# Performance work log

Hardware: AMD Instinct MI355X
Metric: run time of the kernel (lower is better)

The kernel has to match this reference:

```python
import jax, jax.numpy as jnp
import numpy as np

# ---- static config (mirrors build() with the chosen init_kwargs) ----
B, H, W, C = 16, 56, 56, 128
KH, KW = 3, 3          # filter_size
SH, SW = 1, 1          # stride
NF = 256               # n_filters
IN_FEAT = C * KH * KW  # 1152
NNZ = int(1 * 0.2 * IN_FEAT * NF)  # multiple * density * n_parameters = 58982


def _make_indices():
    """Replicates the full='output' sparsity-pattern construction from build()."""
    rng = np.random.default_rng(0)
    per_col = NNZ // NF
    remain = NNZ % NF
    remain_cols = set(rng.choice(NF, remain, replace=False).tolist())
    chunks = []
    for col in rng.permutation(NF):
        k = per_col + (1 if int(col) in remain_cols else 0)
        rows = rng.choice(IN_FEAT, k, replace=False)
        chunks.append(np.stack([rows, np.full(k, col, dtype=np.int64)], axis=1))
    return np.concatenate(chunks, axis=0).astype(np.int32)  # (NNZ, 2) [row, col]


def setup_inputs() -> dict:
    key = jax.random.key(0)
    k1, k2 = jax.random.split(key)
    x = jax.random.normal(k1, (B, H, W, C), dtype=jnp.float32)
    limit = float(np.sqrt(6.0 / (IN_FEAT + NF)))  # glorot_uniform on the sparse values
    kernel = jax.random.uniform(k2, (NNZ,), jnp.float32, -limit, limit)
    bias = jnp.zeros((NF,), jnp.float32)
    indices = jnp.asarray(_make_indices())
    return {"x": x, "kernel": kernel, "bias": bias, "indices": indices}


def _im2col_valid(x):
    # tf.image.extract_patches ordering: patch positions row-major (di, dj),
    # channels fastest -> concatenate C-channel slices in (di, dj) order.
    oh = (H - KH) // SH + 1
    ow = (W - KW) // SW + 1
    cols = [x[:, di:di + oh * SH:SH, dj:dj + ow * SW:SW, :]
            for di in range(KH) for dj in range(KW)]
    return jnp.concatenate(cols, axis=-1), oh, ow  # (B, oh, ow, IN_FEAT)


def reference(x, kernel, bias, indices):
    patches, oh, ow = _im2col_valid(x)
    pm = patches.reshape(-1, IN_FEAT)  # (B*oh*ow, IN_FEAT)
    # Sparse (IN_FEAT, NF) weight: scatter values into a dense matrix
    # (indices are unique by construction, so .add == .set and is grad-safe).
    Wm = jnp.zeros((IN_FEAT, NF), dtype=pm.dtype).at[indices[:, 0], indices[:, 1]].add(kernel)
    out = pm @ Wm + bias            # sparse-dense matmul + bias
    out = jax.nn.relu(out)          # activation
    return out.reshape(B, oh, ow, NF)
```

## Files before the change

kernel.cpp:

```cpp
#include <hip/hip_runtime.h>

typedef unsigned short u16;
typedef __bf16 bf16x8 __attribute__((ext_vector_type(8)));
typedef float f32x4 __attribute__((ext_vector_type(4)));

#define B_   16
#define H_   56
#define W_   56
#define C_   128
#define OH_  54
#define OW_  54
#define NF_  256
#define KF_  1152
#define M_   46656
#define NNZ_ 58982

#define XB_ELEMS (B_*H_*W_*C_)
#define WT_ELEMS (36*4*256*8)

__device__ __forceinline__ u16 f2bf(float f) {
    unsigned u = __float_as_uint(f);
    u += 0x7FFFu + ((u >> 16) & 1u);
    return (u16)(u >> 16);
}

__device__ __forceinline__ void gload16(const void* g, void* l) {
    __builtin_amdgcn_global_load_lds(
        (const __attribute__((address_space(1))) unsigned int*)g,
        (__attribute__((address_space(3))) unsigned int*)l,
        16, 0, 0);
}

__global__ __launch_bounds__(256) void cvt_x_kernel(const float* __restrict__ x,
                                                    u16* __restrict__ xb) {
    int i = (blockIdx.x * 256 + threadIdx.x) * 8;
    float4 v0 = *(const float4*)(x + i);
    float4 v1 = *(const float4*)(x + i + 4);
    union { u16 u[8]; uint4 v; } r;
    r.u[0] = f2bf(v0.x); r.u[1] = f2bf(v0.y); r.u[2] = f2bf(v0.z); r.u[3] = f2bf(v0.w);
    r.u[4] = f2bf(v1.x); r.u[5] = f2bf(v1.y); r.u[6] = f2bf(v1.z); r.u[7] = f2bf(v1.w);
    *(uint4*)(xb + i) = r.v;
}

__global__ __launch_bounds__(256) void scatter_kernel(const float* __restrict__ kv,
                                                      const int* __restrict__ idx,
                                                      u16* __restrict__ wt) {
    int t = blockIdx.x * 256 + threadIdx.x;
    if (t >= NNZ_) return;
    int k   = idx[2*t];
    int col = idx[2*t + 1];
    int kt = k >> 5, ks = (k >> 3) & 3, e = k & 7;
    wt[(kt * 4 + ks) * 2048 + col * 8 + e] = f2bf(kv[t]);
}

__global__ __launch_bounds__(256) void spconv_gemm(const u16* __restrict__ xb,
                                                   const u16* __restrict__ wt,
                                                   const float* __restrict__ bias,
                                                   float* __restrict__ out) {
    __shared__ __align__(16) u16 As[2][64 * 32];
    __shared__ __align__(16) u16 Bs[2][4 * 256 * 8];

    const int t    = threadIdx.x;
    const int lane = t & 63;
    const int wid  = t >> 6;

    const int nwg = gridDim.x;
    const int q = nwg >> 3, r = nwg & 7;
    const int xcd = blockIdx.x & 7, inner = blockIdx.x >> 3;
    const int wg = (xcd < r ? xcd * (q + 1) : r * (q + 1) + (xcd - r) * q) + inner;
    const int m0 = wg * 64;

    const int arow = (wid << 4) | (lane >> 2);
    const int kc   = lane & 3;
    const int kcs  = kc ^ (arow & 3) ^ ((arow >> 2) & 3);
    const int kco  = kcs * 8;
    int mg  = m0 + arow;
    int bb  = mg / (OH_ * OW_);
    int rem = mg % (OH_ * OW_);
    int ii  = rem / OW_;
    int jj  = rem % OW_;
    const u16* a_base = xb + ((bb * H_ + ii) * W_ + jj) * C_;
    const int a_dst = t * 8;
    const int b_dst = t * 8;

    f32x4 acc[4][4];
    const f32x4 zz = {0.f, 0.f, 0.f, 0.f};
#pragma unroll
    for (int i = 0; i < 4; ++i)
#pragma unroll
        for (int j = 0; j < 4; ++j) acc[i][j] = zz;

    const int ks  = lane >> 4;
    const int r16 = lane & 15;
    const int cidx = ks ^ (r16 & 3) ^ ((r16 >> 2) & 3);

#define ISSUE(kn, bi) do {                                                  \
    int g_  = (kn) >> 2;                                                    \
    int di_ = (g_ * 11) >> 5;                                               \
    int dj_ = g_ - 3 * di_;                                                 \
    int aoff_ = (di_ * W_ + dj_) * C_ + ((kn) & 3) * 32 + kco;              \
    gload16(a_base + aoff_, &As[bi][0] + a_dst);                            \
    const u16* bsrc_ = wt + (kn) * 8192 + t * 8;                            \
    gload16(bsrc_,        &Bs[bi][0] + b_dst);                              \
    gload16(bsrc_ + 2048, &Bs[bi][0] + b_dst + 2048);                       \
    gload16(bsrc_ + 4096, &Bs[bi][0] + b_dst + 4096);                       \
    gload16(bsrc_ + 6144, &Bs[bi][0] + b_dst + 6144);                       \
} while (0)

#define COMPUTE(bi) do {                                                    \
    bf16x8 a_[4], b_[4];                                                    \
    _Pragma("unroll")                                                       \
    for (int mf = 0; mf < 4; ++mf)                                          \
        a_[mf] = *(const bf16x8*)(&As[bi][(mf * 16 + r16) * 32 + cidx * 8]);\
    _Pragma("unroll")                                                       \
    for (int nf = 0; nf < 4; ++nf)                                          \
        b_[nf] = *(const bf16x8*)(&Bs[bi][(ks * 256 + wid * 64 + nf * 16 + r16) * 8]); \
    _Pragma("unroll")                                                       \
    for (int mf = 0; mf < 4; ++mf)                                          \
        _Pragma("unroll")                                                   \
        for (int nf = 0; nf < 4; ++nf)                                      \
            acc[mf][nf] = __builtin_amdgcn_mfma_f32_16x16x32_bf16(          \
                a_[mf], b_[nf], acc[mf][nf], 0, 0, 0);                      \
} while (0)

#define WAITVM(n) asm volatile("s_waitcnt vmcnt(" #n ")" ::: "memory")
#define BAR() do { __builtin_amdgcn_s_barrier();                            \
                   asm volatile("" ::: "memory"); } while (0)

    ISSUE(0, 0);
    ISSUE(1, 1);

#pragma unroll
    for (int k = 0; k < 34; ++k) {
        WAITVM(5);
        BAR();
        COMPUTE(k & 1);
        BAR();
        ISSUE(k + 2, k & 1);
    }
    WAITVM(5); BAR(); COMPUTE(0); BAR();
    WAITVM(0); BAR(); COMPUTE(1);

#undef ISSUE
#undef COMPUTE
#undef WAITVM
#undef BAR

    const int rgrp = lane >> 4;
#pragma unroll
    for (int nf = 0; nf < 4; ++nf) {
        int col  = wid * 64 + nf * 16 + r16;
        float bv = bias[col];
#pragma unroll
        for (int mf = 0; mf < 4; ++mf) {
#pragma unroll
            for (int rr = 0; rr < 4; ++rr) {
                int row = m0 + mf * 16 + rgrp * 4 + rr;
                float v = acc[mf][nf][rr] + bv;
                out[row * NF_ + col] = fmaxf(v, 0.f);
            }
        }
    }
}

extern "C" void kernel_launch(void* const* d_in, const int* in_sizes, int n_in,
                              void* d_out, int out_size, void* d_ws, size_t ws_size,
                              hipStream_t stream) {
    const float* x    = (const float*)d_in[0];
    const float* kv   = (const float*)d_in[1];
    const float* bias = (const float*)d_in[2];
    const int*   idx  = (const int*)d_in[3];
    float* out = (float*)d_out;

    u16* xb  = (u16*)d_ws;
    u16* wtp = (u16*)((char*)d_ws + (size_t)XB_ELEMS * 2);

    hipMemsetAsync(wtp, 0, (size_t)WT_ELEMS * 2, stream);
    cvt_x_kernel<<<XB_ELEMS / (256 * 8), 256, 0, stream>>>(x, xb);
    scatter_kernel<<<(NNZ_ + 255) / 256, 256, 0, stream>>>(kv, idx, wtp);
    spconv_gemm<<<M_ / 64, 256, 0, stream>>>(xb, wtp, bias, out);
}
```

Measured before the change: 50.70 us.

## Enlarge GEMM tile to 96 rows with 6 waves and warp-specialized loaders; fuse memset

```diff
diff --git a/kernel.cpp b/kernel.cpp
--- a/kernel.cpp
+++ b/kernel.cpp
@@ -32,7 +32,12 @@
 }
 
 __global__ __launch_bounds__(256) void cvt_x_kernel(const float* __restrict__ x,
-                                                    u16* __restrict__ xb) {
+                                                    u16* __restrict__ xb,
+                                                    u16* __restrict__ wt) {
+    if (blockIdx.x < 144) {
+        uint4 z = {0u, 0u, 0u, 0u};
+        ((uint4*)wt)[blockIdx.x * 256 + threadIdx.x] = z;
+    }
     int i = (blockIdx.x * 256 + threadIdx.x) * 8;
     float4 v0 = *(const float4*)(x + i);
     float4 v1 = *(const float4*)(x + i + 4);
@@ -53,11 +58,11 @@
     wt[(kt * 4 + ks) * 2048 + col * 8 + e] = f2bf(kv[t]);
 }
 
-__global__ __launch_bounds__(256) void spconv_gemm(const u16* __restrict__ xb,
+__global__ __launch_bounds__(384) void spconv_gemm(const u16* __restrict__ xb,
                                                    const u16* __restrict__ wt,
                                                    const float* __restrict__ bias,
                                                    float* __restrict__ out) {
-    __shared__ __align__(16) u16 As[2][64 * 32];
+    __shared__ __align__(16) u16 As[2][96 * 32];
     __shared__ __align__(16) u16 Bs[2][4 * 256 * 8];
 
     const int t    = threadIdx.x;
@@ -68,62 +73,79 @@
     const int q = nwg >> 3, r = nwg & 7;
     const int xcd = blockIdx.x & 7, inner = blockIdx.x >> 3;
     const int wg = (xcd < r ? xcd * (q + 1) : r * (q + 1) + (xcd - r) * q) + inner;
-    const int m0 = wg * 64;
-
-    const int arow = (wid << 4) | (lane >> 2);
-    const int kc   = lane & 3;
-    const int kcs  = kc ^ (arow & 3) ^ ((arow >> 2) & 3);
-    const int kco  = kcs * 8;
-    int mg  = m0 + arow;
-    int bb  = mg / (OH_ * OW_);
-    int rem = mg % (OH_ * OW_);
-    int ii  = rem / OW_;
-    int jj  = rem % OW_;
-    const u16* a_base = xb + ((bb * H_ + ii) * W_ + jj) * C_;
-    const int a_dst = t * 8;
-    const int b_dst = t * 8;
-
-    f32x4 acc[4][4];
+    const int m0 = wg * 96;
+
+    const int u     = t & 127;
+    const int arow0 = u >> 2;
+    const int kc    = u & 3;
+    const int kcs   = kc ^ (arow0 & 3) ^ ((arow0 >> 2) & 3);
+    const int kco   = kcs * 8;
+    const int a_dst0 = u * 8;
+
+    const u16* a_base0;
+    const u16* a_base1;
+    const u16* a_base2;
+    {
+        int mg0 = m0 + arow0;
+#define MKBASE(dst, mg) do {                                   \
+        int bb_  = (mg) / (OH_ * OW_);                         \
+        int rem_ = (mg) % (OH_ * OW_);                         \
+        int ii_  = rem_ / OW_;                                 \
+        int jj_  = rem_ % OW_;                                 \
+        dst = xb + ((bb_ * H_ + ii_) * W_ + jj_) * C_;         \
+    } while (0)
+        MKBASE(a_base0, mg0);
+        MKBASE(a_base1, mg0 + 32);
+        MKBASE(a_base2, mg0 + 64);
+#undef MKBASE
+    }
+
+    f32x4 acc[2][8];
     const f32x4 zz = {0.f, 0.f, 0.f, 0.f};
 #pragma unroll
-    for (int i = 0; i < 4; ++i)
-#pragma unroll
-        for (int j = 0; j < 4; ++j) acc[i][j] = zz;
+    for (int i = 0; i < 2; ++i)
+#pragma unroll
+        for (int j = 0; j < 8; ++j) acc[i][j] = zz;
 
     const int ks  = lane >> 4;
     const int r16 = lane & 15;
     const int cidx = ks ^ (r16 & 3) ^ ((r16 >> 2) & 3);
+    const int wr = wid >> 1;
+    const int wc = wid & 1;
 
 #define ISSUE(kn, bi) do {                                                  \
-    int g_  = (kn) >> 2;                                                    \
-    int di_ = (g_ * 11) >> 5;                                               \
-    int dj_ = g_ - 3 * di_;                                                 \
-    int aoff_ = (di_ * W_ + dj_) * C_ + ((kn) & 3) * 32 + kco;              \
-    gload16(a_base + aoff_, &As[bi][0] + a_dst);                            \
-    const u16* bsrc_ = wt + (kn) * 8192 + t * 8;                            \
-    gload16(bsrc_,        &Bs[bi][0] + b_dst);                              \
-    gload16(bsrc_ + 2048, &Bs[bi][0] + b_dst + 2048);                       \
-    gload16(bsrc_ + 4096, &Bs[bi][0] + b_dst + 4096);                       \
-    gload16(bsrc_ + 6144, &Bs[bi][0] + b_dst + 6144);                       \
+    if (t < 256) {                                                          \
+        const u16* bsrc_ = wt + (kn) * 8192 + t * 8;                        \
+        gload16(bsrc_,        &Bs[bi][0] + t * 8);                          \
+        gload16(bsrc_ + 2048, &Bs[bi][0] + t * 8 + 2048);                   \
+        gload16(bsrc_ + 4096, &Bs[bi][0] + t * 8 + 4096);                   \
+        gload16(bsrc_ + 6144, &Bs[bi][0] + t * 8 + 6144);                   \
+    } else {                                                                \
+        int g_  = (kn) >> 2;                                                \
+        int di_ = (g_ * 11) >> 5;                                           \
+        int dj_ = g_ - 3 * di_;                                             \
+        int aoff_ = (di_ * W_ + dj_) * C_ + ((kn) & 3) * 32 + kco;          \
+        gload16(a_base0 + aoff_, &As[bi][0] + a_dst0);                      \
+        gload16(a_base1 + aoff_, &As[bi][0] + a_dst0 + 1024);               \
+        gload16(a_base2 + aoff_, &As[bi][0] + a_dst0 + 2048);               \
+    }                                                                       \
 } while (0)
 
 #define COMPUTE(bi) do {                                                    \
-    bf16x8 a_[4], b_[4];                                                    \
+    bf16x8 a0_ = *(const bf16x8*)(&As[bi][(wr * 32 + r16) * 32 + cidx * 8]);\
+    bf16x8 a1_ = *(const bf16x8*)(&As[bi][(wr * 32 + 16 + r16) * 32 + cidx * 8]); \
     _Pragma("unroll")                                                       \
-    for (int mf = 0; mf < 4; ++mf)                                          \
-        a_[mf] = *(const bf16x8*)(&As[bi][(mf * 16 + r16) * 32 + cidx * 8]);\
-    _Pragma("unroll")                                                       \
-    for (int nf = 0; nf < 4; ++nf)                                          \
-        b_[nf] = *(const bf16x8*)(&Bs[bi][(ks * 256 + wid * 64 + nf * 16 + r16) * 8]); \
-    _Pragma("unroll")                                                       \
-    for (int mf = 0; mf < 4; ++mf)                                          \
-        _Pragma("unroll")                                                   \
-        for (int nf = 0; nf < 4; ++nf)                                      \
-            acc[mf][nf] = __builtin_amdgcn_mfma_f32_16x16x32_bf16(          \
-                a_[mf], b_[nf], acc[mf][nf], 0, 0, 0);                      \
+    for (int nf = 0; nf < 8; ++nf) {                                        \
+        bf16x8 b_ = *(const bf16x8*)(&Bs[bi][(ks * 256 + wc * 128 + nf * 16 + r16) * 8]); \
+        acc[0][nf] = __builtin_amdgcn_mfma_f32_16x16x32_bf16(a0_, b_, acc[0][nf], 0, 0, 0); \
+        acc[1][nf] = __builtin_amdgcn_mfma_f32_16x16x32_bf16(a1_, b_, acc[1][nf], 0, 0, 0); \
+    }                                                                       \
 } while (0)
 
-#define WAITVM(n) asm volatile("s_waitcnt vmcnt(" #n ")" ::: "memory")
+#define WAITVM(nb, na) do {                                                 \
+    if (wid < 4) { asm volatile("s_waitcnt vmcnt(" #nb ")" ::: "memory"); } \
+    else         { asm volatile("s_waitcnt vmcnt(" #na ")" ::: "memory"); } \
+} while (0)
 #define BAR() do { __builtin_amdgcn_s_barrier();                            \
                    asm volatile("" ::: "memory"); } while (0)
 
@@ -132,14 +154,14 @@
 
 #pragma unroll
     for (int k = 0; k < 34; ++k) {
-        WAITVM(5);
+        WAITVM(4, 3);
         BAR();
         COMPUTE(k & 1);
         BAR();
         ISSUE(k + 2, k & 1);
     }
-    WAITVM(5); BAR(); COMPUTE(0); BAR();
-    WAITVM(0); BAR(); COMPUTE(1);
+    WAITVM(4, 3); BAR(); COMPUTE(0); BAR();
+    WAITVM(0, 0); BAR(); COMPUTE(1);
 
 #undef ISSUE
 #undef COMPUTE
@@ -148,14 +170,14 @@
 
     const int rgrp = lane >> 4;
 #pragma unroll
-    for (int nf = 0; nf < 4; ++nf) {
-        int col  = wid * 64 + nf * 16 + r16;
+    for (int nf = 0; nf < 8; ++nf) {
+        int col  = wc * 128 + nf * 16 + r16;
         float bv = bias[col];
 #pragma unroll
-        for (int mf = 0; mf < 4; ++mf) {
+        for (int mf = 0; mf < 2; ++mf) {
 #pragma unroll
             for (int rr = 0; rr < 4; ++rr) {
-                int row = m0 + mf * 16 + rgrp * 4 + rr;
+                int row = m0 + wr * 32 + mf * 16 + rgrp * 4 + rr;
                 float v = acc[mf][nf][rr] + bv;
                 out[row * NF_ + col] = fmaxf(v, 0.f);
             }
@@ -175,8 +197,7 @@
     u16* xb  = (u16*)d_ws;
     u16* wtp = (u16*)((char*)d_ws + (size_t)XB_ELEMS * 2);
 
-    hipMemsetAsync(wtp, 0, (size_t)WT_ELEMS * 2, stream);
-    cvt_x_kernel<<<XB_ELEMS / (256 * 8), 256, 0, stream>>>(x, xb);
+    cvt_x_kernel<<<XB_ELEMS / (256 * 8), 256, 0, stream>>>(x, xb, wtp);
     scatter_kernel<<<(NNZ_ + 255) / 256, 256, 0, stream>>>(kv, idx, wtp);
-    spconv_gemm<<<M_ / 64, 256, 0, stream>>>(xb, wtp, bias, out);
-}
+    spconv_gemm<<<M_ / 96, 384, 0, stream>>>(xb, wtp, bias, out);
+}
```

After: 53.10 us. 4.7% more time.

## Split GEMM tile into 64x128 halves and fold weight memset into convert kernel

Applied to the files above, without the earlier changes.

```diff
diff --git a/kernel.cpp b/kernel.cpp
--- a/kernel.cpp
+++ b/kernel.cpp
@@ -32,7 +32,12 @@
 }
 
 __global__ __launch_bounds__(256) void cvt_x_kernel(const float* __restrict__ x,
-                                                    u16* __restrict__ xb) {
+                                                    u16* __restrict__ xb,
+                                                    u16* __restrict__ wt) {
+    if (blockIdx.x < 144) {
+        uint4 z = {0u, 0u, 0u, 0u};
+        ((uint4*)wt)[blockIdx.x * 256 + threadIdx.x] = z;
+    }
     int i = (blockIdx.x * 256 + threadIdx.x) * 8;
     float4 v0 = *(const float4*)(x + i);
     float4 v1 = *(const float4*)(x + i + 4);
@@ -58,7 +63,7 @@
                                                    const float* __restrict__ bias,
                                                    float* __restrict__ out) {
     __shared__ __align__(16) u16 As[2][64 * 32];
-    __shared__ __align__(16) u16 Bs[2][4 * 256 * 8];
+    __shared__ __align__(16) u16 Bs[2][4 * 128 * 8];
 
     const int t    = threadIdx.x;
     const int lane = t & 63;
@@ -68,10 +73,12 @@
     const int q = nwg >> 3, r = nwg & 7;
     const int xcd = blockIdx.x & 7, inner = blockIdx.x >> 3;
     const int wg = (xcd < r ? xcd * (q + 1) : r * (q + 1) + (xcd - r) * q) + inner;
-    const int m0 = wg * 64;
+    const int mi = wg >> 1;
+    const int ni = wg & 1;
+    const int m0 = mi * 64;
 
-    const int arow = (wid << 4) | (lane >> 2);
-    const int kc   = lane & 3;
+    const int arow = t >> 2;
+    const int kc   = t & 3;
     const int kcs  = kc ^ (arow & 3) ^ ((arow >> 2) & 3);
     const int kco  = kcs * 8;
     int mg  = m0 + arow;
@@ -81,18 +88,24 @@
     int jj  = rem % OW_;
     const u16* a_base = xb + ((bb * H_ + ii) * W_ + jj) * C_;
     const int a_dst = t * 8;
-    const int b_dst = t * 8;
 
-    f32x4 acc[4][4];
+    const u16* b_src0 = wt + (t >> 7) * 2048 + ni * 1024 + (t & 127) * 8;
+    const u16* b_src1 = b_src0 + 2 * 2048;
+    const int b_dst0 = t * 8;
+    const int b_dst1 = t * 8 + 2048;
+
+    f32x4 acc[2][4];
     const f32x4 zz = {0.f, 0.f, 0.f, 0.f};
 #pragma unroll
-    for (int i = 0; i < 4; ++i)
+    for (int i = 0; i < 2; ++i)
 #pragma unroll
         for (int j = 0; j < 4; ++j) acc[i][j] = zz;
 
     const int ks  = lane >> 4;
     const int r16 = lane & 15;
     const int cidx = ks ^ (r16 & 3) ^ ((r16 >> 2) & 3);
+    const int wr = wid >> 1;
+    const int wc = wid & 1;
 
 #define ISSUE(kn, bi) do {                                                  \
     int g_  = (kn) >> 2;                                                    \
@@ -100,27 +113,19 @@
     int dj_ = g_ - 3 * di_;                                                 \
     int aoff_ = (di_ * W_ + dj_) * C_ + ((kn) & 3) * 32 + kco;              \
     gload16(a_base + aoff_, &As[bi][0] + a_dst);                            \
-    const u16* bsrc_ = wt + (kn) * 8192 + t * 8;                            \
-    gload16(bsrc_,        &Bs[bi][0] + b_dst);                              \
-    gload16(bsrc_ + 2048, &Bs[bi][0] + b_dst + 2048);                       \
-    gload16(bsrc_ + 4096, &Bs[bi][0] + b_dst + 4096);                       \
-    gload16(bsrc_ + 6144, &Bs[bi][0] + b_dst + 6144);                       \
+    gload16(b_src0 + (kn) * 8192, &Bs[bi][0] + b_dst0);                     \
+    gload16(b_src1 + (kn) * 8192, &Bs[bi][0] + b_dst1);                     \
 } while (0)
 
 #define COMPUTE(bi) do {                                                    \
-    bf16x8 a_[4], b_[4];                                                    \
+    bf16x8 a0_ = *(const bf16x8*)(&As[bi][(wr * 32 + r16) * 32 + cidx * 8]);\
+    bf16x8 a1_ = *(const bf16x8*)(&As[bi][(wr * 32 + 16 + r16) * 32 + cidx * 8]); \
     _Pragma("unroll")                                                       \
-    for (int mf = 0; mf < 4; ++mf)                                          \
-        a_[mf] = *(const bf16x8*)(&As[bi][(mf * 16 + r16) * 32 + cidx * 8]);\
-    _Pragma("unroll")                                                       \
-    for (int nf = 0; nf < 4; ++nf)                                          \
-        b_[nf] = *(const bf16x8*)(&Bs[bi][(ks * 256 + wid * 64 + nf * 16 + r16) * 8]); \
-    _Pragma("unroll")                                                       \
-    for (int mf = 0; mf < 4; ++mf)                                          \
-        _Pragma("unroll")                                                   \
-        for (int nf = 0; nf < 4; ++nf)                                      \
-            acc[mf][nf] = __builtin_amdgcn_mfma_f32_16x16x32_bf16(          \
-                a_[mf], b_[nf], acc[mf][nf], 0, 0, 0);                      \
+    for (int nf = 0; nf < 4; ++nf) {                                        \
+        bf16x8 b_ = *(const bf16x8*)(&Bs[bi][(ks * 128 + wc * 64 + nf * 16 + r16) * 8]); \
+        acc[0][nf] = __builtin_amdgcn_mfma_f32_16x16x32_bf16(a0_, b_, acc[0][nf], 0, 0, 0); \
+        acc[1][nf] = __builtin_amdgcn_mfma_f32_16x16x32_bf16(a1_, b_, acc[1][nf], 0, 0, 0); \
+    }                                                                       \
 } while (0)
 
 #define WAITVM(n) asm volatile("s_waitcnt vmcnt(" #n ")" ::: "memory")
@@ -132,13 +137,13 @@
 
 #pragma unroll
     for (int k = 0; k < 34; ++k) {
-        WAITVM(5);
+        WAITVM(3);
         BAR();
         COMPUTE(k & 1);
         BAR();
         ISSUE(k + 2, k & 1);
     }
-    WAITVM(5); BAR(); COMPUTE(0); BAR();
+    WAITVM(3); BAR(); COMPUTE(0); BAR();
     WAITVM(0); BAR(); COMPUTE(1);
 
 #undef ISSUE
@@ -149,13 +154,13 @@
     const int rgrp = lane >> 4;
 #pragma unroll
     for (int nf = 0; nf < 4; ++nf) {
-        int col  = wid * 64 + nf * 16 + r16;
+        int col  = ni * 128 + wc * 64 + nf * 16 + r16;
         float bv = bias[col];
 #pragma unroll
-        for (int mf = 0; mf < 4; ++mf) {
+        for (int mf = 0; mf < 2; ++mf) {
 #pragma unroll
             for (int rr = 0; rr < 4; ++rr) {
-                int row = m0 + mf * 16 + rgrp * 4 + rr;
+                int row = m0 + wr * 32 + mf * 16 + rgrp * 4 + rr;
                 float v = acc[mf][nf][rr] + bv;
                 out[row * NF_ + col] = fmaxf(v, 0.f);
             }
@@ -175,8 +180,7 @@
     u16* xb  = (u16*)d_ws;
     u16* wtp = (u16*)((char*)d_ws + (size_t)XB_ELEMS * 2);
 
-    hipMemsetAsync(wtp, 0, (size_t)WT_ELEMS * 2, stream);
-    cvt_x_kernel<<<XB_ELEMS / (256 * 8), 256, 0, stream>>>(x, xb);
+    cvt_x_kernel<<<XB_ELEMS / (256 * 8), 256, 0, stream>>>(x, xb, wtp);
     scatter_kernel<<<(NNZ_ + 255) / 256, 256, 0, stream>>>(kv, idx, wtp);
-    spconv_gemm<<<M_ / 64, 256, 0, stream>>>(xb, wtp, bias, out);
+    spconv_gemm<<<(M_ / 64) * 2, 256, 0, stream>>>(xb, wtp, bias, out);
 }
```

Result: no change. 49.73 us (-1.9%).
